# Kernel optimization log

Hardware: AMD Instinct MI355X
Metric: run time of the kernel (lower is better)

Reference implementation:

```python
import jax, jax.numpy as jnp
import numpy as np

B, C, H, W = 4, 1024, 14, 14
L = 80          # num labels / graph nodes
WD = 300        # word embedding dim
INTER = 1024    # semantic intermediary dim
OUT = 2048      # output_dim
TIME_STEP = 3


def setup_inputs() -> dict:
    key = jax.random.key(0)
    ks = jax.random.split(key, 24)
    s = 0.02  # weight scale to keep gates/tanh in sane range
    return {
        "img_feature_map": jax.random.normal(ks[0], (B, C, H, W), jnp.float32),
        "word_embedding": jax.random.normal(ks[1], (L, WD), jnp.float32),
        "adjacency": jax.random.uniform(ks[2], (L, L), jnp.float32) / L,
        "fc1_w": jax.random.normal(ks[3], (INTER, C), jnp.float32) * s,
        "fc2_w": jax.random.normal(ks[4], (INTER, WD), jnp.float32) * s,
        "fc3_w": jax.random.normal(ks[5], (INTER, INTER), jnp.float32) * s,
        "fc3_b": jnp.zeros((INTER,), jnp.float32),
        "fca_w": jax.random.normal(ks[6], (1, INTER), jnp.float32) * s,
        "fca_b": jnp.zeros((1,), jnp.float32),
        "w3": jax.random.normal(ks[7], (C, 2 * C), jnp.float32) * s,
        "b3": jnp.zeros((C,), jnp.float32),
        "u3": jax.random.normal(ks[8], (C, C), jnp.float32) * s,
        "u3b": jnp.zeros((C,), jnp.float32),
        "w4": jax.random.normal(ks[9], (C, 2 * C), jnp.float32) * s,
        "b4": jnp.zeros((C,), jnp.float32),
        "w5": jax.random.normal(ks[10], (C, 2 * C), jnp.float32) * s,
        "b5": jnp.zeros((C,), jnp.float32),
        "u5": jax.random.normal(ks[11], (C, C), jnp.float32) * s,
        "u5b": jnp.zeros((C,), jnp.float32),
        "fco_w": jax.random.normal(ks[12], (OUT, 2 * C), jnp.float32) * s,
        "fco_b": jnp.zeros((OUT,), jnp.float32),
    }


def _semantic(fmap, word_emb, fc1_w, fc2_w, fc3_w, fc3_b, fca_w, fca_b):
    # Faithful to torch: view(-1, C) on a contiguous (B,C,H,W) tensor is a raw
    # row-major reinterpret (NOT a BHWC transpose). jnp.reshape matches.
    b, c, h, w = fmap.shape
    x = fmap.reshape(-1, c)                                   # (B*H*W, C)
    f_wh = x @ fc1_w.T                                        # (N, INTER)
    f_wd = word_emb @ fc2_w.T                                 # (L, INTER)
    lb = jnp.tanh(f_wh[:, None, :] * f_wd[None, :, :])        # (N, L, INTER)
    lb = lb @ fc3_w.T + fc3_b                                 # (N, L, INTER)
    coeff = lb @ fca_w.T + fca_b                              # (N, L, 1)
    coeff = coeff.reshape(b, L, h * w)                        # torch .view semantics
    coeff = jax.nn.softmax(coeff, axis=2)
    coeff = coeff.reshape(b, h, w, L)
    fmap_bhwc = fmap.reshape(b, h, w, c)                      # raw reinterpret, as torch
    return jnp.einsum('bhwl,bhwc->blc', coeff, fmap_bhwc)     # (B, L, C)


def _ggnn(nodes, adj, w3, b3, u3, u3b, w4, b4, w5, b5, u5, u5b):
    for _ in range(TIME_STEP):
        a = jnp.einsum('nm,bmd->bnd', adj, nodes)             # in == out matrix
        av = jnp.concatenate([a, a], axis=-1)                 # (B, L, 2C)
        u3x = nodes @ u3.T + u3b
        z = jax.nn.sigmoid(av @ w3.T + b3 + u3x)
        r = jax.nn.sigmoid(av @ w4.T + b4 + u3x)              # torch bug: reuses fc_eq3_u
        hcand = jnp.tanh(av @ w5.T + b5 + (r * nodes) @ u5.T + u5b)
        nodes = (1.0 - z) * nodes + z * hcand
    return nodes


def reference(img_feature_map, word_embedding, adjacency,
              fc1_w, fc2_w, fc3_w, fc3_b, fca_w, fca_b,
              w3, b3, u3, u3b, w4, b4, w5, b5, u5, u5b,
              fco_w, fco_b):
    g = _semantic(img_feature_map, word_embedding,
                  fc1_w, fc2_w, fc3_w, fc3_b, fca_w, fca_b)   # (B, L, C)
    nodes = _ggnn(g, adjacency, w3, b3, u3, u3b, w4, b4, w5, b5, u5, u5b)
    feat = jnp.concatenate([nodes, g], axis=-1)               # (B, L, 2C)
    out = jnp.tanh(feat @ fco_w.T + fco_b)                    # (B, L, OUT)
    return out
```

## Files before the change

### kernel.cpp

```cpp
#include <hip/hip_runtime.h>
#include <hip/hip_bf16.h>

#define LL 80
#define NPIX 784
#define PBATCH 15680

#define DI __device__ __forceinline__

typedef short s8v __attribute__((ext_vector_type(8)));
typedef short short4v __attribute__((ext_vector_type(4)));
typedef float f32x4 __attribute__((ext_vector_type(4)));

DI float b2f(__hip_bfloat16 x) { return __bfloat162float(x); }
DI float s2f(short h) { return __uint_as_float(((unsigned int)(unsigned short)h) << 16); }

DI short f2b(float x) {
    unsigned int b = __float_as_uint(x);
    b += 0x7fffu + ((b >> 16) & 1u);
    return (short)(b >> 16);
}

template <int F> DI float LD(const void* p, int i) {
    if (F) return ((const float*)p)[i];
    return b2f(((const __hip_bfloat16*)p)[i]);
}

DI float fast_tanh(float x) {
    float e = __expf(2.0f * x);
    return 1.0f - 2.0f / (e + 1.0f);
}
DI float fast_sigmoid(float x) { return 1.0f / (1.0f + __expf(-x)); }

__global__ __launch_bounds__(256) void detect_dtype(const void* probe, int n, int* flag) {
    __shared__ int bad;
    if (threadIdx.x == 0) bad = 0;
    __syncthreads();
    int c = 0;
    for (int i = threadIdx.x; i < n; i += 256) {
        float v = b2f(((const __hip_bfloat16*)probe)[i]);
        if (!(fabsf(v) < 1000.0f)) c++;
    }
    if (c) atomicAdd(&bad, c);
    __syncthreads();
    if (threadIdx.x == 0) *flag = (bad > 8) ? 1 : 0;
}

DI void cvt_part(int f, const void* src, short* __restrict__ dst, int blk, int n) {
    int i0 = (blk * 256 + threadIdx.x) * 4;
    if (i0 >= n) return;
    if (f) {
        float4 v = *(const float4*)((const float*)src + i0);
        short4v o = { f2b(v.x), f2b(v.y), f2b(v.z), f2b(v.w) };
        *(short4v*)(dst + i0) = o;
    } else {
        *(short4v*)(dst + i0) = *(const short4v*)((const short*)src + i0);
    }
}

DI void cvt_pad(int f, const void* src, short* __restrict__ dst, int blk, int n) {
    int i0 = (blk * 256 + threadIdx.x) * 4;
    if (i0 >= n) return;
    int row = i0 / 320;
    int k = i0 - row * 320;
    short4v o = {0, 0, 0, 0};
    if (k < 300) {
        if (f) {
            float4 v = *(const float4*)((const float*)src + row * 300 + k);
            o.x = f2b(v.x); o.y = f2b(v.y); o.z = f2b(v.z); o.w = f2b(v.w);
        } else {
            o = *(const short4v*)((const short*)src + row * 300 + k);
        }
    }
    *(short4v*)(dst + i0) = o;
}

DI void wcat_part(int f, const void* w3, const void* w4, const void* w5, const void* u3,
                  short* __restrict__ wcat, int blk) {
    int i0 = (blk * 256 + threadIdx.x) * 4;
    int nr = i0 >> 10, k = i0 & 1023;
    int j = nr >> 10, r = nr & 1023;
    const void* W = (j == 0) ? w3 : (j == 1) ? w4 : (j == 2) ? w5 : u3;
    float4 v;
    if (j < 3) {
        if (f) {
            float4 x = *(const float4*)((const float*)W + r * 2048 + k);
            float4 y = *(const float4*)((const float*)W + r * 2048 + 1024 + k);
            v.x = x.x + y.x; v.y = x.y + y.y; v.z = x.z + y.z; v.w = x.w + y.w;
        } else {
            const short* Ws = (const short*)W;
            short4v x = *(const short4v*)(Ws + r * 2048 + k);
            short4v y = *(const short4v*)(Ws + r * 2048 + 1024 + k);
            v.x = s2f(x.x) + s2f(y.x); v.y = s2f(x.y) + s2f(y.y);
            v.z = s2f(x.z) + s2f(y.z); v.w = s2f(x.w) + s2f(y.w);
        }
    } else {
        if (f) v = *(const float4*)((const float*)W + r * 1024 + k);
        else {
            short4v x = *(const short4v*)((const short*)W + r * 1024 + k);
            v.x = s2f(x.x); v.y = s2f(x.y); v.z = s2f(x.z); v.w = s2f(x.w);
        }
    }
    short4v o = { f2b(v.x), f2b(v.y), f2b(v.z), f2b(v.w) };
    *(short4v*)(wcat + i0) = o;
}

template <int F>
DI void prep_upart(const void* fc3_w, const void* fca_w,
                   float* __restrict__ u_part, int blk) {
    int kseg = blk >> 4, jseg = blk & 15;
    int k = kseg * 256 + threadIdx.x;
    int j0 = jseg * 64;
    float acc = 0.f;
    for (int j = j0; j < j0 + 64; j++)
        acc += LD<F>(fca_w, j) * LD<F>(fc3_w, j * 1024 + k);
    u_part[jseg * 1024 + k] = acc;
}

template <int F>
DI void prep_c0(const void* fc3_b, const void* fca_w, const void* fca_b,
                float* c0, float* red) {
    float acc = 0.f;
    for (int j = threadIdx.x; j < 1024; j += 256)
        acc += LD<F>(fc3_b, j) * LD<F>(fca_w, j);
    red[threadIdx.x] = acc;
    __syncthreads();
    for (int s = 128; s > 0; s >>= 1) {
        if (threadIdx.x < s) red[threadIdx.x] += red[threadIdx.x + s];
        __syncthreads();
    }
    if (threadIdx.x == 0) {
        float v = red[0] + LD<F>(fca_b, 0);
        c0[0] = v;
        c0[1] = v;
    }
}

__global__ __launch_bounds__(256) void mega_prep(
    const int* flag,
    const void* fmap, const void* fc1_w, const void* u5w,
    const void* w3, const void* w4, const void* w5, const void* u3,
    const void* fc3_w, const void* fc3_b, const void* fca_w, const void* fca_b,
    const void* word, const void* fc2_w,
    short* fmap_b, short* fc1w_b, short* u5w_b, short* wcat_b,
    short* word_b, short* fc2w_b,
    float* u_part, float* c0) {
    __shared__ float red[256];
    int f = *flag;
    int bid = blockIdx.x;
    if      (bid < 784)  cvt_part(f, fmap,  fmap_b, bid,        802816);
    else if (bid < 1808) cvt_part(f, fc1_w, fc1w_b, bid - 784,  1048576);
    else if (bid < 2832) cvt_part(f, u5w,   u5w_b,  bid - 1808, 1048576);
    else if (bid < 6928) wcat_part(f, w3, w4, w5, u3, wcat_b, bid - 2832);
    else if (bid < 6992) {
        if (f) prep_upart<1>(fc3_w, fca_w, u_part, bid - 6928);
        else   prep_upart<0>(fc3_w, fca_w, u_part, bid - 6928);
    } else if (bid == 6992) {
        if (f) prep_c0<1>(fc3_b, fca_w, fca_b, c0, red);
        else   prep_c0<0>(fc3_b, fca_w, fca_b, c0, red);
    }
    else if (bid < 7018) cvt_pad(f, word,  word_b, bid - 6993, 25600);
    else                 cvt_pad(f, fc2_w, fc2w_b, bid - 7018, 327680);
}

__global__ __launch_bounds__(256) void cvt_k(const int* flag, const void* src,
                                             short* __restrict__ dst, int n) {
    cvt_part(*flag, src, dst, blockIdx.x, n);
}

DI void mcore_b(const short* __restrict__ A, int lda,
                const short* __restrict__ B, int ldb,
                float* __restrict__ C, int ldc,
                int M, int kb, int ke, int m0, int n0) {
    __shared__ short As[4][64][8];
    __shared__ short Ws[4][64][8];
    const int tid = threadIdx.x;
    const int wv = tid >> 6, lane = tid & 63;
    const int mA = tid & 63, qA = tid >> 6;
    f32x4 acc[4] = {};

    for (int k0 = kb; k0 < ke; k0 += 32) {
        s8v va = {0,0,0,0,0,0,0,0};
        int gm = m0 + mA;
        if (gm < M) va = *(const s8v*)(A + gm * lda + k0 + 8 * qA);
        *(s8v*)&As[mA >> 4][(mA & 15) | (qA << 4)][0] = va;
        s8v vb = *(const s8v*)(B + (n0 + mA) * ldb + k0 + 8 * qA);
        *(s8v*)&Ws[mA >> 4][(mA & 15) | (qA << 4)][0] = vb;
        __syncthreads();
        s8v af = *(const s8v*)&As[wv][lane][0];
#pragma unroll
        for (int nf = 0; nf < 4; nf++) {
            s8v bf = *(const s8v*)&Ws[nf][lane][0];
            acc[nf] = __builtin_amdgcn_mfma_f32_16x16x32_bf16(af, bf, acc[nf], 0, 0, 0);
        }
        __syncthreads();
    }

    const int q = lane >> 4, cc = lane & 15;
#pragma unroll
    for (int nf = 0; nf < 4; nf++) {
        int n = n0 + 16 * nf + cc;
#pragma unroll
        for (int r = 0; r < 4; r++) {
            int m = m0 + 16 * wv + q * 4 + r;
            if (m < M) C[m * ldc + n] = acc[nf][r];
        }
    }
}

__global__ __launch_bounds__(256) void mfma_sem(
    const short* __restrict__ fmap_b, const short* __restrict__ fc1w_b,
    const short* __restrict__ word_b, const short* __restrict__ fc2w_b,
    const float* __restrict__ u_part, float* __restrict__ u, float* __restrict__ c0,
    float* __restrict__ fhP, float* __restrict__ f_wd) {
    int bid = blockIdx.x;
    if (bid < 416) {
        int z = bid / 208, r = bid % 208;
        int by = r / 16, bx = r % 16;
        mcore_b(fmap_b, 1024, fc1w_b, 1024, fhP + z * 802816, 1024,
                NPIX, z * 512, z * 512 + 512, by * 64, bx * 64);
    } else if (bid < 448) {
        int r = bid - 416;
        int by = r >> 4, bx = r & 15;
        mcore_b(word_b, 320, fc2w_b, 320, f_wd, 1024,
                80, 0, 320, by * 64, bx * 64);
    } else {
        __shared__ float red[256];
        int k = (bid - 448) * 256 + threadIdx.x;
        float a = 0.f;
#pragma unroll
        for (int si = 0; si < 16; si++) a += u_part[si * 1024 + k];
        u[k] = a;
        red[threadIdx.x] = a;
        __syncthreads();
        for (int st = 128; st > 0; st >>= 1) {
            if (threadIdx.x < st) red[threadIdx.x] += red[threadIdx.x + st];
            __syncthreads();
        }
        if (threadIdx.x == 0) atomicAdd(c0 + 1, red[0]);
    }
}

__global__ __launch_bounds__(256) void mfma_gate(
    const short* __restrict__ a_b, const short* __restrict__ nodes_b,
    const short* __restrict__ wcat_b, float* __restrict__ gP) {
    int z = blockIdx.z;
    const short* A = (blockIdx.x >= 48) ? nodes_b : a_b;
    mcore_b(A, 1024, wcat_b, 1024, gP + z * 1310720, 4096,
            320, z * 512, z * 512 + 512, blockIdx.y * 64, blockIdx.x * 64);
}

__global__ __launch_bounds__(256) void mfma_u5(
    const short* __restrict__ rn_b, const short* __restrict__ u5w_b,
    float* __restrict__ u5P) {
    int z = blockIdx.z;
    mcore_b(rn_b, 1024, u5w_b, 1024, u5P + z * 327680, 1024,
            320, z * 256, z * 256 + 256, blockIdx.y * 64, blockIdx.x * 64);
}

__global__ __launch_bounds__(256) void mfma_fin(
    const short* __restrict__ nodes_b, const short* __restrict__ g_b,
    const short* __restrict__ fcow_b, float* __restrict__ finP) {
    int z = blockIdx.z;
    const short* A = z ? (g_b - 1024) : nodes_b;
    mcore_b(A, 1024, fcow_b, 2048, finP + z * 655360, 2048,
            320, z * 1024, z * 1024 + 1024, blockIdx.y * 64, blockIdx.x * 64);
}

__global__ void fin_combine(const int* flag, const float* __restrict__ finP,
                            const void* fco_b, void* out, int n) {
    int i4 = (blockIdx.x * 256 + threadIdx.x) * 4;
    if (i4 >= n) return;
    int c = i4 & 2047;
    float4 p0 = *(const float4*)(finP + i4);
    float4 p1 = *(const float4*)(finP + 655360 + i4);
    int f = *flag;
    float v0 = fast_tanh(p0.x + p1.x + (f ? LD<1>(fco_b, c)   : LD<0>(fco_b, c)));
    float v1 = fast_tanh(p0.y + p1.y + (f ? LD<1>(fco_b, c+1) : LD<0>(fco_b, c+1)));
    float v2 = fast_tanh(p0.z + p1.z + (f ? LD<1>(fco_b, c+2) : LD<0>(fco_b, c+2)));
    float v3 = fast_tanh(p0.w + p1.w + (f ? LD<1>(fco_b, c+3) : LD<0>(fco_b, c+3)));
    if (f) {
        float4 o = {v0, v1, v2, v3};
        *(float4*)((float*)out + i4) = o;
    } else {
        short4v o = { f2b(v0), f2b(v1), f2b(v2), f2b(v3) };
        *(short4v*)((short*)out + i4) = o;
    }
}

__global__ __launch_bounds__(256) void coeff_kernel(
    const float* __restrict__ fhP, const float* __restrict__ f_wd,
    const float* __restrict__ u, const float* __restrict__ c0p,
    float* __restrict__ s) {
    __shared__ float h2s[4][1024];
    __shared__ float us[1024];
    const float K2 = 2.8853900817779268f;
    int t = threadIdx.x;
    int n0 = blockIdx.x * 4;
#pragma unroll
    for (int r = 0; r < 4; r++) {
        int n = n0 + r;
        float4 a0 = *(const float4*)(fhP + n * 1024 + t * 4);
        float4 a1 = *(const float4*)(fhP + 802816 + n * 1024 + t * 4);
        float4 hv = {K2 * (a0.x + a1.x), K2 * (a0.y + a1.y),
                     K2 * (a0.z + a1.z), K2 * (a0.w + a1.w)};
        *(float4*)&h2s[r][t * 4] = hv;
    }
    *(float4*)&us[t * 4] = *(const float4*)(u + t * 4);
    __syncthreads();
    float c0U = c0p[1];
    int wave = t >> 6, lane = t & 63;
    int b = n0 / 196, hw0 = n0 % 196;
    int l0 = blockIdx.y * 20;
    for (int l = l0 + wave; l < l0 + 20; l += 4) {
        const float4* fd4 = (const float4*)(f_wd + l * 1024);
        float p0 = 0.f, p1 = 0.f, p2 = 0.f, p3 = 0.f;
#pragma unroll
        for (int j = 0; j < 4; j++) {
            int idx = lane + j * 64;
            float4 d  = fd4[idx];
            float4 uu = *(const float4*)&us[idx * 4];
            float4 h0 = *(const float4*)&h2s[0][idx * 4];
            float4 h1 = *(const float4*)&h2s[1][idx * 4];
            float4 h2 = *(const float4*)&h2s[2][idx * 4];
            float4 h3 = *(const float4*)&h2s[3][idx * 4];
#define TERM(P, H) \
    P += uu.x * __builtin_amdgcn_rcpf(1.0f + __builtin_amdgcn_exp2f(H.x * d.x)); \
    P += uu.y * __builtin_amdgcn_rcpf(1.0f + __builtin_amdgcn_exp2f(H.y * d.y)); \
    P += uu.z * __builtin_amdgcn_rcpf(1.0f + __builtin_amdgcn_exp2f(H.z * d.z)); \
    P += uu.w * __builtin_amdgcn_rcpf(1.0f + __builtin_amdgcn_exp2f(H.w * d.w));
            TERM(p0, h0) TERM(p1, h1) TERM(p2, h2) TERM(p3, h3)
#undef TERM
        }
        for (int off = 32; off > 0; off >>= 1) {
            p0 += __shfl_down(p0, off);
            p1 += __shfl_down(p1, off);
            p2 += __shfl_down(p2, off);
            p3 += __shfl_down(p3, off);
        }
        if (lane == 0) {
            float* sp = s + b * PBATCH + hw0 * LL + l;
            sp[0]      = c0U - 2.f * p0;
            sp[LL]     = c0U - 2.f * p1;
            sp[2 * LL] = c0U - 2.f * p2;
            sp[3 * LL] = c0U - 2.f * p3;
        }
    }
}

__global__ __launch_bounds__(64) void softmax196(float* __restrict__ s) {
    float* p = s + blockIdx.x * 196;
    int lane = threadIdx.x;
    float v[4];
    float mx = -1e30f;
#pragma unroll
    for (int i = 0; i < 4; i++) {
        int idx = lane + i * 64;
        v[i] = (idx < 196) ? p[idx] : -1e30f;
        mx = fmaxf(mx, v[i]);
    }
    for (int off = 32; off > 0; off >>= 1) mx = fmaxf(mx, __shfl_down(mx, off));
    mx = __shfl(mx, 0);
    float sum = 0.f;
#pragma unroll
    for (int i = 0; i < 4; i++) {
        int idx = lane + i * 64;
        if (idx < 196) { v[i] = __expf(v[i] - mx); sum += v[i]; }
    }
    for (int off = 32; off > 0; off >>= 1) sum += __shfl_down(sum, off);
    sum = __shfl(sum, 0);
    float inv = 1.f / sum;
#pragma unroll
    for (int i = 0; i < 4; i++) {
        int idx = lane + i * 64;
        if (idx < 196) p[idx] = v[i] * inv;
    }
}

__global__ __launch_bounds__(256) void g_kernel(
    const float* __restrict__ s, const short* __restrict__ fmap_b,
    float* __restrict__ nodes, short* __restrict__ nodes_b, short* __restrict__ g_b) {
    int bl = blockIdx.x;
    int b = bl / LL, l = bl % LL;
    __shared__ float co[196];
    for (int i = threadIdx.x; i < 196; i += 256)
        co[i] = s[b * PBATCH + i * LL + l];
    __syncthreads();
    int c4 = threadIdx.x * 4;
    const short* base = fmap_b + b * 196 * 1024 + c4;
    float a0 = 0.f, a1 = 0.f, a2 = 0.f, a3 = 0.f;
    for (int hw = 0; hw < 196; hw++) {
        short4v v = *(const short4v*)(base + hw * 1024);
        float w = co[hw];
        a0 += w * s2f(v.x); a1 += w * s2f(v.y);
        a2 += w * s2f(v.z); a3 += w * s2f(v.w);
    }
    int o = bl * 1024 + c4;
    float4 fa = {a0, a1, a2, a3};
    *(float4*)(nodes + o) = fa;
    short4v bb = { f2b(a0), f2b(a1), f2b(a2), f2b(a3) };
    *(short4v*)(nodes_b + o) = bb;
    *(short4v*)(g_b + o) = bb;
}

template <int F>
DI void adj_core(float* arw, const void* adj, const float* nodes, short* a_b) {
    int bl = blockIdx.x;
    int b = bl / LL, l = bl % LL;
    if (threadIdx.x < LL) arw[threadIdx.x] = LD<F>(adj, l * LL + threadIdx.x);
    __syncthreads();
    int c4 = threadIdx.x * 4;
    const float* nb = nodes + b * LL * 1024 + c4;
    float a0 = 0.f, a1 = 0.f, a2 = 0.f, a3 = 0.f;
    for (int m = 0; m < LL; m++) {
        float am = arw[m];
        float4 nd = *(const float4*)(nb + m * 1024);
        a0 += am * nd.x; a1 += am * nd.y; a2 += am * nd.z; a3 += am * nd.w;
    }
    short4v bb = { f2b(a0), f2b(a1), f2b(a2), f2b(a3) };
    *(short4v*)(a_b + bl * 1024 + c4) = bb;
}

__global__ __launch_bounds__(256) void adj_kernel(
    const int* flag, const void* adj, const float* nodes, short* a_b) {
    __shared__ float arw[LL];
    if (*flag) adj_core<1>(arw, adj, nodes, a_b);
    else       adj_core<0>(arw, adj, nodes, a_b);
}

template <int F>
DI void ew_r_core(const float* gP, const float* nodes,
                  const void* b4, const void* u3b, short* rn_b, int i4) {
    int m = i4 >> 10, c = i4 & 1023;
    int base = m * 4096;
    float4 r0 = *(const float4*)(gP + base + 1024 + c);
    float4 r1 = *(const float4*)(gP + 1310720 + base + 1024 + c);
    float4 x0 = *(const float4*)(gP + base + 3072 + c);
    float4 x1 = *(const float4*)(gP + 1310720 + base + 3072 + c);
    float4 nd = *(const float4*)(nodes + i4);
    short4v o;
    o.x = f2b(fast_sigmoid(r0.x + r1.x + x0.x + x1.x + LD<F>(b4, c)   + LD<F>(u3b, c))   * nd.x);
    o.y = f2b(fast_sigmoid(r0.y + r1.y + x0.y + x1.y + LD<F>(b4, c+1) + LD<F>(u3b, c+1)) * nd.y);
    o.z = f2b(fast_sigmoid(r0.z + r1.z + x0.z + x1.z + LD<F>(b4, c+2) + LD<F>(u3b, c+2)) * nd.z);
    o.w = f2b(fast_sigmoid(r0.w + r1.w + x0.w + x1.w + LD<F>(b4, c+3) + LD<F>(u3b, c+3)) * nd.w);
    *(short4v*)(rn_b + i4) = o;
}

__global__ void ew_r(const int* flag, const float* gP, const float* nodes,
                     const void* b4, const void* u3b, short* rn_b, int n) {
    int i4 = (blockIdx.x * 256 + threadIdx.x) * 4;
    if (i4 >= n) return;
    if (*flag) ew_r_core<1>(gP, nodes, b4, u3b, rn_b, i4);
    else       ew_r_core<0>(gP, nodes, b4, u3b, rn_b, i4);
}

template <int F>
DI void ewu(const float* gP, const float* u5P,
            const void* b3, const void* u3b, const void* b5, const void* u5b,
            float* nodes, short* nodes_b, int i4) {
    int m = i4 >> 10, c = i4 & 1023;
    int base = m * 4096;
    float4 z0 = *(const float4*)(gP + base + c);
    float4 z1 = *(const float4*)(gP + 1310720 + base + c);
    float4 h0 = *(const float4*)(gP + base + 2048 + c);
    float4 h1 = *(const float4*)(gP + 1310720 + base + 2048 + c);
    float4 x0 = *(const float4*)(gP + base + 3072 + c);
    float4 x1 = *(const float4*)(gP + 1310720 + base + 3072 + c);
    float4 u0 = *(const float4*)(u5P + i4);
    float4 u1 = *(const float4*)(u5P + 327680 + i4);
    float4 u2 = *(const float4*)(u5P + 655360 + i4);
    float4 u3v = *(const float4*)(u5P + 983040 + i4);
    float4 nd = *(const float4*)(nodes + i4);
    float4 out;
#define EWU1(CH, CO) { \
    float z = fast_sigmoid(z0.CH + z1.CH + x0.CH + x1.CH + LD<F>(b3, c+CO) + LD<F>(u3b, c+CO)); \
    float h = fast_tanh(h0.CH + h1.CH + u0.CH + u1.CH + u2.CH + u3v.CH + LD<F>(b5, c+CO) + LD<F>(u5b, c+CO)); \
    out.CH = (1.f - z) * nd.CH + z * h; }
    EWU1(x, 0) EWU1(y, 1) EWU1(z, 2) EWU1(w, 3)
#undef EWU1
    *(float4*)(nodes + i4) = out;
    short4v bb = { f2b(out.x), f2b(out.y), f2b(out.z), f2b(out.w) };
    *(short4v*)(nodes_b + i4) = bb;
}

__global__ void ew_upd(const int* flag, const float* gP, const float* u5P,
                       const void* b3, const void* u3b, const void* b5, const void* u5b,
                       float* nodes, short* nodes_b, int n) {
    int i4 = (blockIdx.x * 256 + threadIdx.x) * 4;
    if (i4 >= n) return;
    if (*flag) ewu<1>(gP, u5P, b3, u3b, b5, u5b, nodes, nodes_b, i4);
    else       ewu<0>(gP, u5P, b3, u3b, b5, u5b, nodes, nodes_b, i4);
}

extern "C" void kernel_launch(void* const* d_in, const int* in_sizes, int n_in,
                              void* d_out, int out_size, void* d_ws, size_t ws_size,
                              hipStream_t stream) {
    const void* fmap  = d_in[0];
    const void* word  = d_in[1];
    const void* adjm  = d_in[2];
    const void* fc1_w = d_in[3];
    const void* fc2_w = d_in[4];
    const void* fc3_w = d_in[5];
    const void* fc3_b = d_in[6];
    const void* fca_w = d_in[7];
    const void* fca_b = d_in[8];
    const void* w3    = d_in[9];
    const void* b3    = d_in[10];
    const void* u3    = d_in[11];
    const void* u3b   = d_in[12];
    const void* w4    = d_in[13];
    const void* b4    = d_in[14];
    const void* w5    = d_in[15];
    const void* b5    = d_in[16];
    const void* u5    = d_in[17];
    const void* u5b   = d_in[18];
    const void* fco_w = d_in[19];
    const void* fco_b = d_in[20];

    int*   flag    = (int*)d_ws;
    float* P       = (float*)d_ws + 16;
    float* nodes   = P;                       P += 327680;
    short* nodes_b = (short*)P;               P += 163840;
    short* g_b     = (short*)P;               P += 163840;
    short* a_b     = (short*)P;               P += 163840;
    short* rn_b    = (short*)P;               P += 163840;
    short* u5w_b   = (short*)P;               P += 524288;
    short* wcat_b  = (short*)P;               P += 2097152;
    float* R       = P;
    float* fhP    = R;
    float* f_wd   = R + 1605632;
    float* u_part = f_wd + 81920;
    float* u      = u_part + 16384;
    float* c0     = u + 1024;
    float* s      = c0 + 16;
    short* fmap_b = (short*)(s + 62720);
    short* fc1w_b = fmap_b + 802816;
    short* word_b = fc1w_b + 1048576;
    short* fc2w_b = word_b + 25600;
    float* gP     = R;
    float* u5P    = R + 2621440;
    float* finP   = R;
    short* fcow_b = (short*)(R + 1310720);

    detect_dtype<<<1, 256, 0, stream>>>(fc1_w, 4096, flag);

    mega_prep<<<7338, 256, 0, stream>>>(flag, fmap, fc1_w, u5,
                                        w3, w4, w5, u3,
                                        fc3_w, fc3_b, fca_w, fca_b,
                                        word, fc2_w,
                                        fmap_b, fc1w_b, u5w_b, wcat_b,
                                        word_b, fc2w_b, u_part, c0);

    mfma_sem<<<452, 256, 0, stream>>>(fmap_b, fc1w_b, word_b, fc2w_b,
                                      u_part, u, c0, fhP, f_wd);
    coeff_kernel<<<dim3(196, 4), 256, 0, stream>>>(fhP, f_wd, u, c0, s);
    softmax196<<<320, 64, 0, stream>>>(s);
    g_kernel<<<320, 256, 0, stream>>>(s, fmap_b, nodes, nodes_b, g_b);

    for (int t = 0; t < 3; t++) {
        adj_kernel<<<320, 256, 0, stream>>>(flag, adjm, nodes, a_b);
        mfma_gate<<<dim3(64, 5, 2), 256, 0, stream>>>(a_b, nodes_b, wcat_b, gP);
        ew_r<<<320, 256, 0, stream>>>(flag, gP, nodes, b4, u3b, rn_b, 327680);
        mfma_u5<<<dim3(16, 5, 4), 256, 0, stream>>>(rn_b, u5w_b, u5P);
        ew_upd<<<320, 256, 0, stream>>>(flag, gP, u5P, b3, u3b, b5, u5b,
                                        nodes, nodes_b, 327680);
    }

    cvt_k<<<4096, 256, 0, stream>>>(flag, fco_w, fcow_b, 4194304);
    mfma_fin<<<dim3(32, 5, 2), 256, 0, stream>>>(nodes_b, g_b, fcow_b, finP);
    fin_combine<<<640, 256, 0, stream>>>(flag, finP, fco_b, d_out, 655360);
}
```

Before: 341.2 us.

## Fuse GRU gate GEMM with sigmoid epilogue and concatenate K over adj and nodes

Reorders the combined gate weight so the z and r columns for the same output channels share one tile, and concatenates the adjacency and nodes inputs along K (2048). This lets one GEMM compute full pre-activations and apply sigmoid, biases and r*nodes in its epilogue. It removes the ew_r kernel, the split-K partial buffers and the big gP traffic, and ew_upd gets simpler. It also moves the fco_w bf16 conversion into the prep megakernel when the workspace has room, at the cost of a larger weight buffer and a less parallel gate grid (240 blocks without split-K).

```diff
diff --git a/kernel.cpp b/kernel.cpp
--- a/kernel.cpp
+++ b/kernel.cpp
@@ -24,6 +24,7 @@
     if (F) return ((const float*)p)[i];
     return b2f(((const __hip_bfloat16*)p)[i]);
 }
+DI float LDf(int f, const void* p, int i) { return f ? ((const float*)p)[i] : b2f(((const __hip_bfloat16*)p)[i]); }
 
 DI float fast_tanh(float x) {
     float e = __expf(2.0f * x);
@@ -74,30 +75,49 @@
     *(short4v*)(dst + i0) = o;
 }
 
-DI void wcat_part(int f, const void* w3, const void* w4, const void* w5, const void* u3,
-                  short* __restrict__ wcat, int blk) {
+DI void wcat2_part(int f, const void* w3, const void* w4, const void* w5, const void* u3,
+                   short* __restrict__ wcat, int blk) {
     int i0 = (blk * 256 + threadIdx.x) * 4;
-    int nr = i0 >> 10, k = i0 & 1023;
-    int j = nr >> 10, r = nr & 1023;
-    const void* W = (j == 0) ? w3 : (j == 1) ? w4 : (j == 2) ? w5 : u3;
-    float4 v;
-    if (j < 3) {
-        if (f) {
-            float4 x = *(const float4*)((const float*)W + r * 2048 + k);
-            float4 y = *(const float4*)((const float*)W + r * 2048 + 1024 + k);
-            v.x = x.x + y.x; v.y = x.y + y.y; v.z = x.z + y.z; v.w = x.w + y.w;
+    int j = i0 >> 11, k = i0 & 2047;
+    float4 v = {0.f, 0.f, 0.f, 0.f};
+    if (j < 2048) {
+        int slot = (j >> 4) & 3, cl = j & 15;
+        int c = (j >> 6) * 32 + ((slot >> 1) << 4) + cl;
+        if (k < 1024) {
+            const void* W = (slot & 1) ? w4 : w3;
+            if (f) {
+                float4 x = *(const float4*)((const float*)W + c * 2048 + k);
+                float4 y = *(const float4*)((const float*)W + c * 2048 + 1024 + k);
+                v.x = x.x + y.x; v.y = x.y + y.y; v.z = x.z + y.z; v.w = x.w + y.w;
+            } else {
+                const short* Ws = (const short*)W;
+                short4v x = *(const short4v*)(Ws + c * 2048 + k);
+                short4v y = *(const short4v*)(Ws + c * 2048 + 1024 + k);
+                v.x = s2f(x.x) + s2f(y.x); v.y = s2f(x.y) + s2f(y.y);
+                v.z = s2f(x.z) + s2f(y.z); v.w = s2f(x.w) + s2f(y.w);
+            }
         } else {
-            const short* Ws = (const short*)W;
-            short4v x = *(const short4v*)(Ws + r * 2048 + k);
-            short4v y = *(const short4v*)(Ws + r * 2048 + 1024 + k);
-            v.x = s2f(x.x) + s2f(y.x); v.y = s2f(x.y) + s2f(y.y);
-            v.z = s2f(x.z) + s2f(y.z); v.w = s2f(x.w) + s2f(y.w);
+            int kk = k - 1024;
+            if (f) v = *(const float4*)((const float*)u3 + c * 1024 + kk);
+            else {
+                short4v x = *(const short4v*)((const short*)u3 + c * 1024 + kk);
+                v.x = s2f(x.x); v.y = s2f(x.y); v.z = s2f(x.z); v.w = s2f(x.w);
+            }
         }
     } else {
-        if (f) v = *(const float4*)((const float*)W + r * 1024 + k);
-        else {
-            short4v x = *(const short4v*)((const short*)W + r * 1024 + k);
-            v.x = s2f(x.x); v.y = s2f(x.y); v.z = s2f(x.z); v.w = s2f(x.w);
+        int c = j - 2048;
+        if (k < 1024) {
+            if (f) {
+                float4 x = *(const float4*)((const float*)w5 + c * 2048 + k);
+                float4 y = *(const float4*)((const float*)w5 + c * 2048 + 1024 + k);
+                v.x = x.x + y.x; v.y = x.y + y.y; v.z = x.z + y.z; v.w = x.w + y.w;
+            } else {
+                const short* Ws = (const short*)w5;
+                short4v x = *(const short4v*)(Ws + c * 2048 + k);
+                short4v y = *(const short4v*)(Ws + c * 2048 + 1024 + k);
+                v.x = s2f(x.x) + s2f(y.x); v.y = s2f(x.y) + s2f(y.y);
+                v.z = s2f(x.z) + s2f(y.z); v.w = s2f(x.w) + s2f(y.w);
+            }
         }
     }
     short4v o = { f2b(v.x), f2b(v.y), f2b(v.z), f2b(v.w) };
@@ -140,9 +160,9 @@
     const void* fmap, const void* fc1_w, const void* u5w,
     const void* w3, const void* w4, const void* w5, const void* u3,
     const void* fc3_w, const void* fc3_b, const void* fca_w, const void* fca_b,
-    const void* word, const void* fc2_w,
+    const void* word, const void* fc2_w, const void* fco_w,
     short* fmap_b, short* fc1w_b, short* u5w_b, short* wcat_b,
-    short* word_b, short* fc2w_b,
+    short* word_b, short* fc2w_b, short* fcow_b,
     float* u_part, float* c0) {
     __shared__ float red[256];
     int f = *flag;
@@ -150,16 +170,17 @@
     if      (bid < 784)  cvt_part(f, fmap,  fmap_b, bid,        802816);
     else if (bid < 1808) cvt_part(f, fc1_w, fc1w_b, bid - 784,  1048576);
     else if (bid < 2832) cvt_part(f, u5w,   u5w_b,  bid - 1808, 1048576);
-    else if (bid < 6928) wcat_part(f, w3, w4, w5, u3, wcat_b, bid - 2832);
-    else if (bid < 6992) {
-        if (f) prep_upart<1>(fc3_w, fca_w, u_part, bid - 6928);
-        else   prep_upart<0>(fc3_w, fca_w, u_part, bid - 6928);
-    } else if (bid == 6992) {
+    else if (bid < 8976) wcat2_part(f, w3, w4, w5, u3, wcat_b, bid - 2832);
+    else if (bid < 9040) {
+        if (f) prep_upart<1>(fc3_w, fca_w, u_part, bid - 8976);
+        else   prep_upart<0>(fc3_w, fca_w, u_part, bid - 8976);
+    } else if (bid == 9040) {
         if (f) prep_c0<1>(fc3_b, fca_w, fca_b, c0, red);
         else   prep_c0<0>(fc3_b, fca_w, fca_b, c0, red);
     }
-    else if (bid < 7018) cvt_pad(f, word,  word_b, bid - 6993, 25600);
-    else                 cvt_pad(f, fc2_w, fc2w_b, bid - 7018, 327680);
+    else if (bid < 9066) cvt_pad(f, word,  word_b, bid - 9041, 25600);
+    else if (bid < 9386) cvt_pad(f, fc2_w, fc2w_b, bid - 9066, 327680);
+    else                 cvt_part(f, fco_w, fcow_b, bid - 9386, 4194304);
 }
 
 __global__ __launch_bounds__(256) void cvt_k(const int* flag, const void* src,
@@ -240,13 +261,75 @@
     }
 }
 
-__global__ __launch_bounds__(256) void mfma_gate(
+__global__ __launch_bounds__(256) void mfma_gateF(
+    const int* flag,
     const short* __restrict__ a_b, const short* __restrict__ nodes_b,
-    const short* __restrict__ wcat_b, float* __restrict__ gP) {
-    int z = blockIdx.z;
-    const short* A = (blockIdx.x >= 48) ? nodes_b : a_b;
-    mcore_b(A, 1024, wcat_b, 1024, gP + z * 1310720, 4096,
-            320, z * 512, z * 512 + 512, blockIdx.y * 64, blockIdx.x * 64);
+    const short* __restrict__ wcat_b, const float* __restrict__ nodes,
+    const void* b3, const void* b4, const void* u3b,
+    const void* b5, const void* u5b,
+    float* __restrict__ zs, float* __restrict__ hp, short* __restrict__ rn_b) {
+    __shared__ short As[4][64][8];
+    __shared__ short Ws[4][64][8];
+    const int tid = threadIdx.x;
+    const int wv = tid >> 6, lane = tid & 63;
+    const int mA = tid & 63, qA = tid >> 6;
+    const int bn = blockIdx.x;
+    const int m0 = blockIdx.y * 64;
+    const int n0 = bn * 64;
+    const int ke = (bn < 32) ? 2048 : 1024;
+    f32x4 acc[4] = {};
+
+    for (int k0 = 0; k0 < ke; k0 += 32) {
+        const short* Arow = (k0 < 1024)
+            ? (a_b + (m0 + mA) * 1024 + k0)
+            : (nodes_b + (m0 + mA) * 1024 + (k0 - 1024));
+        s8v va = *(const s8v*)(Arow + 8 * qA);
+        *(s8v*)&As[mA >> 4][(mA & 15) | (qA << 4)][0] = va;
+        s8v vb = *(const s8v*)(wcat_b + (n0 + mA) * 2048 + k0 + 8 * qA);
+        *(s8v*)&Ws[mA >> 4][(mA & 15) | (qA << 4)][0] = vb;
+        __syncthreads();
+        s8v af = *(const s8v*)&As[wv][lane][0];
+#pragma unroll
+        for (int nf = 0; nf < 4; nf++) {
+            s8v bf = *(const s8v*)&Ws[nf][lane][0];
+            acc[nf] = __builtin_amdgcn_mfma_f32_16x16x32_bf16(af, bf, acc[nf], 0, 0, 0);
+        }
+        __syncthreads();
+    }
+
+    const int q = lane >> 4, cc = lane & 15;
+    const int f = *flag;
+    if (bn < 32) {
+        int c0c = bn * 32 + cc;
+        int c1c = c0c + 16;
+        float bz0 = LDf(f, b3, c0c) + LDf(f, u3b, c0c);
+        float br0 = LDf(f, b4, c0c) + LDf(f, u3b, c0c);
+        float bz1 = LDf(f, b3, c1c) + LDf(f, u3b, c1c);
+        float br1 = LDf(f, b4, c1c) + LDf(f, u3b, c1c);
+#pragma unroll
+        for (int r = 0; r < 4; r++) {
+            int m = m0 + 16 * wv + q * 4 + r;
+            float z0v = fast_sigmoid(acc[0][r] + bz0);
+            float r0v = fast_sigmoid(acc[1][r] + br0);
+            float z1v = fast_sigmoid(acc[2][r] + bz1);
+            float r1v = fast_sigmoid(acc[3][r] + br1);
+            zs[m * 1024 + c0c] = z0v;
+            zs[m * 1024 + c1c] = z1v;
+            rn_b[m * 1024 + c0c] = f2b(r0v * nodes[m * 1024 + c0c]);
+            rn_b[m * 1024 + c1c] = f2b(r1v * nodes[m * 1024 + c1c]);
+        }
+    } else {
+#pragma unroll
+        for (int nf = 0; nf < 4; nf++) {
+            int c = (bn - 32) * 64 + 16 * nf + cc;
+            float bb = LDf(f, b5, c) + LDf(f, u5b, c);
+#pragma unroll
+            for (int r = 0; r < 4; r++) {
+                int m = m0 + 16 * wv + q * 4 + r;
+                hp[m * 1024 + c] = acc[nf][r] + bb;
+            }
+        }
+    }
 }
 
 __global__ __launch_bounds__(256) void mfma_u5(
@@ -427,68 +510,26 @@
     else       adj_core<0>(arw, adj, nodes, a_b);
 }
 
-template <int F>
-DI void ew_r_core(const float* gP, const float* nodes,
-                  const void* b4, const void* u3b, short* rn_b, int i4) {
-    int m = i4 >> 10, c = i4 & 1023;
-    int base = m * 4096;
-    float4 r0 = *(const float4*)(gP + base + 1024 + c);
-    float4 r1 = *(const float4*)(gP + 1310720 + base + 1024 + c);
-    float4 x0 = *(const float4*)(gP + base + 3072 + c);
-    float4 x1 = *(const float4*)(gP + 1310720 + base + 3072 + c);
-    float4 nd = *(const float4*)(nodes + i4);
-    short4v o;
-    o.x = f2b(fast_sigmoid(r0.x + r1.x + x0.x + x1.x + LD<F>(b4, c)   + LD<F>(u3b, c))   * nd.x);
-    o.y = f2b(fast_sigmoid(r0.y + r1.y + x0.y + x1.y + LD<F>(b4, c+1) + LD<F>(u3b, c+1)) * nd.y);
-    o.z = f2b(fast_sigmoid(r0.z + r1.z + x0.z + x1.z + LD<F>(b4, c+2) + LD<F>(u3b, c+2)) * nd.z);
-    o.w = f2b(fast_sigmoid(r0.w + r1.w + x0.w + x1.w + LD<F>(b4, c+3) + LD<F>(u3b, c+3)) * nd.w);
-    *(short4v*)(rn_b + i4) = o;
-}
-
-__global__ void ew_r(const int* flag, const float* gP, const float* nodes,
-                     const void* b4, const void* u3b, short* rn_b, int n) {
+__global__ void ew_upd(const float* __restrict__ zs, const float* __restrict__ hp,
+                       const float* __restrict__ u5P,
+                       float* __restrict__ nodes, short* __restrict__ nodes_b, int n) {
     int i4 = (blockIdx.x * 256 + threadIdx.x) * 4;
     if (i4 >= n) return;
-    if (*flag) ew_r_core<1>(gP, nodes, b4, u3b, rn_b, i4);
-    else       ew_r_core<0>(gP, nodes, b4, u3b, rn_b, i4);
-}
-
-template <int F>
-DI void ewu(const float* gP, const float* u5P,
-            const void* b3, const void* u3b, const void* b5, const void* u5b,
-            float* nodes, short* nodes_b, int i4) {
-    int m = i4 >> 10, c = i4 & 1023;
-    int base = m * 4096;
-    float4 z0 = *(const float4*)(gP + base + c);
-    float4 z1 = *(const float4*)(gP + 1310720 + base + c);
-    float4 h0 = *(const float4*)(gP + base + 2048 + c);
-    float4 h1 = *(const float4*)(gP + 1310720 + base + 2048 + c);
-    float4 x0 = *(const float4*)(gP + base + 3072 + c);
-    float4 x1 = *(const float4*)(gP + 1310720 + base + 3072 + c);
+    float4 zv = *(const float4*)(zs + i4);
+    float4 hv = *(const float4*)(hp + i4);
     float4 u0 = *(const float4*)(u5P + i4);
     float4 u1 = *(const float4*)(u5P + 327680 + i4);
     float4 u2 = *(const float4*)(u5P + 655360 + i4);
     float4 u3v = *(const float4*)(u5P + 983040 + i4);
     float4 nd = *(const float4*)(nodes + i4);
     float4 out;
-#define EWU1(CH, CO) { \
-    float z = fast_sigmoid(z0.CH + z1.CH + x0.CH + x1.CH + LD<F>(b3, c+CO) + LD<F>(u3b, c+CO)); \
-    float h = fast_tanh(h0.CH + h1.CH + u0.CH + u1.CH + u2.CH + u3v.CH + LD<F>(b5, c+CO) + LD<F>(u5b, c+CO)); \
-    out.CH = (1.f - z) * nd.CH + z * h; }
-    EWU1(x, 0) EWU1(y, 1) EWU1(z, 2) EWU1(w, 3)
-#undef EWU1
+    out.x = (1.f - zv.x) * nd.x + zv.x * fast_tanh(hv.x + u0.x + u1.x + u2.x + u3v.x);
+    out.y = (1.f - zv.y) * nd.y + zv.y * fast_tanh(hv.y + u0.y + u1.y + u2.y + u3v.y);
+    out.z = (1.f - zv.z) * nd.z + zv.z * fast_tanh(hv.z + u0.z + u1.z + u2.z + u3v.z);
+    out.w = (1.f - zv.w) * nd.w + zv.w * fast_tanh(hv.w + u0.w + u1.w + u2.w + u3v.w);
     *(float4*)(nodes + i4) = out;
     short4v bb = { f2b(out.x), f2b(out.y), f2b(out.z), f2b(out.w) };
     *(short4v*)(nodes_b + i4) = bb;
-}
-
-__global__ void ew_upd(const int* flag, const float* gP, const float* u5P,
-                       const void* b3, const void* u3b, const void* b5, const void* u5b,
-                       float* nodes, short* nodes_b, int n) {
-    int i4 = (blockIdx.x * 256 + threadIdx.x) * 4;
-    if (i4 >= n) return;
-    if (*flag) ewu<1>(gP, u5P, b3, u3b, b5, u5b, nodes, nodes_b, i4);
-    else       ewu<0>(gP, u5P, b3, u3b, b5, u5b, nodes, nodes_b, i4);
 }
 
 extern "C" void kernel_launch(void* const* d_in, const int* in_sizes, int n_in,
@@ -524,7 +565,12 @@
     short* a_b     = (short*)P;               P += 163840;
     short* rn_b    = (short*)P;               P += 163840;
     short* u5w_b   = (short*)P;               P += 524288;
-    short* wcat_b  = (short*)P;               P += 2097152;
+    short* wcat_b  = (short*)P;               P += 3145728;
+    size_t base_f = 16 + 327680 + 163840*4 + 524288 + 3145728;
+    size_t need_ded = (base_f + 2097152 + 2870032) * 4;
+    bool fco_ded = ws_size >= need_ded;
+    short* fcow_ded = (short*)P;
+    if (fco_ded) P += 2097152;
     float* R       = P;
     float* fhP    = R;
     float* f_wd   = R + 1605632;
@@ -536,19 +582,19 @@
     short* fc1w_b = fmap_b + 802816;
     short* word_b = fc1w_b + 1048576;
     short* fc2w_b = word_b + 25600;
-    float* gP     = R;
-    float* u5P    = R + 2621440;
+    float* zs     = R;
+    float* hp     = R + 327680;
+    float* u5P    = R + 655360;
     float* finP   = R;
-    short* fcow_b = (short*)(R + 1310720);
+    short* fcow_b = fco_ded ? fcow_ded : wcat_b;
 
     detect_dtype<<<1, 256, 0, stream>>>(fc1_w, 4096, flag);
 
-    mega_prep<<<7338, 256, 0, stream>>>(flag, fmap, fc1_w, u5,
-                                        w3, w4, w5, u3,
-                                        fc3_w, fc3_b, fca_w, fca_b,
-                                        word, fc2_w,
-                                        fmap_b, fc1w_b, u5w_b, wcat_b,
-                                        word_b, fc2w_b, u_part, c0);
+    mega_prep<<<fco_ded ? 13482 : 9386, 256, 0, stream>>>(
+        flag, fmap, fc1_w, u5, w3, w4, w5, u3,
+        fc3_w, fc3_b, fca_w, fca_b, word, fc2_w, fco_w,
+        fmap_b, fc1w_b, u5w_b, wcat_b, word_b, fc2w_b, fcow_ded,
+        u_part, c0);
 
     mfma_sem<<<452, 256, 0, stream>>>(fmap_b, fc1w_b, word_b, fc2w_b,
                                       u_part, u, c0, fhP, f_wd);
@@ -558,14 +604,15 @@
 
     for (int t = 0; t < 3; t++) {
         adj_kernel<<<320, 256, 0, stream>>>(flag, adjm, nodes, a_b);
-        mfma_gate<<<dim3(64, 5, 2), 256, 0, stream>>>(a_b, nodes_b, wcat_b, gP);
-        ew_r<<<320, 256, 0, stream>>>(flag, gP, nodes, b4, u3b, rn_b, 327680);
+        mfma_gateF<<<dim3(48, 5), 256, 0, stream>>>(flag, a_b, nodes_b, wcat_b,
+                                                    nodes, b3, b4, u3b, b5, u5b,
+                                                    zs, hp, rn_b);
         mfma_u5<<<dim3(16, 5, 4), 256, 0, stream>>>(rn_b, u5w_b, u5P);
-        ew_upd<<<320, 256, 0, stream>>>(flag, gP, u5P, b3, u3b, b5, u5b,
-                                        nodes, nodes_b, 327680);
-    }
-
-    cvt_k<<<4096, 256, 0, stream>>>(flag, fco_w, fcow_b, 4194304);
+        ew_upd<<<320, 256, 0, stream>>>(zs, hp, u5P, nodes, nodes_b, 327680);
+    }
+
+    if (!fco_ded)
+        cvt_k<<<4096, 256, 0, stream>>>(flag, fco_w, fcow_b, 4194304);
     mfma_fin<<<dim3(32, 5, 2), 256, 0, stream>>>(nodes_b, g_b, fcow_b, finP);
     fin_combine<<<640, 256, 0, stream>>>(flag, finP, fco_b, d_out, 655360);
 }
```

After: 390.7 us. 14.5% more time.

## Fuse final GEMM split-K with bias-tanh epilogue and fold fco_w conversion into prep

Applied to the files above, without the earlier changes.

The fco_w bf16 conversion moves into the mega_prep launch with a dedicated workspace buffer, which removes one kernel launch. The final projection becomes a single kernel that runs the whole K=2048 reduction, switching its A source from nodes to g at the midpoint, and applies bias and tanh in the epilogue. This drops the split-K partial buffer and the separate combine kernel. In exchange the final GEMM has only 160 blocks, each with a K loop twice as long, so it exposes less parallelism.

```diff
diff --git a/kernel.cpp b/kernel.cpp
--- a/kernel.cpp
+++ b/kernel.cpp
@@ -24,6 +24,7 @@
     if (F) return ((const float*)p)[i];
     return b2f(((const __hip_bfloat16*)p)[i]);
 }
+DI float LDf(int f, const void* p, int i) { return f ? ((const float*)p)[i] : b2f(((const __hip_bfloat16*)p)[i]); }
 
 DI float fast_tanh(float x) {
     float e = __expf(2.0f * x);
@@ -140,9 +141,9 @@
     const void* fmap, const void* fc1_w, const void* u5w,
     const void* w3, const void* w4, const void* w5, const void* u3,
     const void* fc3_w, const void* fc3_b, const void* fca_w, const void* fca_b,
-    const void* word, const void* fc2_w,
+    const void* word, const void* fc2_w, const void* fco_w,
     short* fmap_b, short* fc1w_b, short* u5w_b, short* wcat_b,
-    short* word_b, short* fc2w_b,
+    short* word_b, short* fc2w_b, short* fcow_b,
     float* u_part, float* c0) {
     __shared__ float red[256];
     int f = *flag;
@@ -159,12 +160,8 @@
         else   prep_c0<0>(fc3_b, fca_w, fca_b, c0, red);
     }
     else if (bid < 7018) cvt_pad(f, word,  word_b, bid - 6993, 25600);
-    else                 cvt_pad(f, fc2_w, fc2w_b, bid - 7018, 327680);
-}
-
-__global__ __launch_bounds__(256) void cvt_k(const int* flag, const void* src,
-                                             short* __restrict__ dst, int n) {
-    cvt_part(*flag, src, dst, blockIdx.x, n);
+    else if (bid < 7338) cvt_pad(f, fc2_w, fc2w_b, bid - 7018, 327680);
+    else                 cvt_part(f, fco_w, fcow_b, bid - 7338, 4194304);
 }
 
 DI void mcore_b(const short* __restrict__ A, int lda,
@@ -204,6 +201,33 @@
             int m = m0 + 16 * wv + q * 4 + r;
             if (m < M) C[m * ldc + n] = acc[nf][r];
         }
+    }
+}
+
+DI void mcore_acc(const short* __restrict__ Aa, const short* __restrict__ Ab, int ksw,
+                  int lda, const short* __restrict__ B, int ldb,
+                  int kb, int ke, int m0, int n0, f32x4* acc) {
+    __shared__ short As[4][64][8];
+    __shared__ short Ws[4][64][8];
+    const int tid = threadIdx.x;
+    const int wv = tid >> 6, lane = tid & 63;
+    const int mA = tid & 63, qA = tid >> 6;
+
+    for (int k0 = kb; k0 < ke; k0 += 32) {
+        const short* Ar = (k0 < ksw) ? (Aa + (m0 + mA) * lda + k0)
+                                     : (Ab + (m0 + mA) * lda + (k0 - ksw));
+        s8v va = *(const s8v*)(Ar + 8 * qA);
+        *(s8v*)&As[mA >> 4][(mA & 15) | (qA << 4)][0] = va;
+        s8v vb = *(const s8v*)(B + (n0 + mA) * ldb + k0 + 8 * qA);
+        *(s8v*)&Ws[mA >> 4][(mA & 15) | (qA << 4)][0] = vb;
+        __syncthreads();
+        s8v af = *(const s8v*)&As[wv][lane][0];
+#pragma unroll
+        for (int nf = 0; nf < 4; nf++) {
+            s8v bf = *(const s8v*)&Ws[nf][lane][0];
+            acc[nf] = __builtin_amdgcn_mfma_f32_16x16x32_bf16(af, bf, acc[nf], 0, 0, 0);
+        }
+        __syncthreads();
     }
 }
 
@@ -257,33 +281,28 @@
             320, z * 256, z * 256 + 256, blockIdx.y * 64, blockIdx.x * 64);
 }
 
-__global__ __launch_bounds__(256) void mfma_fin(
+__global__ __launch_bounds__(256) void mfma_finC(
+    const int* flag,
     const short* __restrict__ nodes_b, const short* __restrict__ g_b,
-    const short* __restrict__ fcow_b, float* __restrict__ finP) {
-    int z = blockIdx.z;
-    const short* A = z ? (g_b - 1024) : nodes_b;
-    mcore_b(A, 1024, fcow_b, 2048, finP + z * 655360, 2048,
-            320, z * 1024, z * 1024 + 1024, blockIdx.y * 64, blockIdx.x * 64);
-}
-
-__global__ void fin_combine(const int* flag, const float* __restrict__ finP,
-                            const void* fco_b, void* out, int n) {
-    int i4 = (blockIdx.x * 256 + threadIdx.x) * 4;
-    if (i4 >= n) return;
-    int c = i4 & 2047;
-    float4 p0 = *(const float4*)(finP + i4);
-    float4 p1 = *(const float4*)(finP + 655360 + i4);
-    int f = *flag;
-    float v0 = fast_tanh(p0.x + p1.x + (f ? LD<1>(fco_b, c)   : LD<0>(fco_b, c)));
-    float v1 = fast_tanh(p0.y + p1.y + (f ? LD<1>(fco_b, c+1) : LD<0>(fco_b, c+1)));
-    float v2 = fast_tanh(p0.z + p1.z + (f ? LD<1>(fco_b, c+2) : LD<0>(fco_b, c+2)));
-    float v3 = fast_tanh(p0.w + p1.w + (f ? LD<1>(fco_b, c+3) : LD<0>(fco_b, c+3)));
-    if (f) {
-        float4 o = {v0, v1, v2, v3};
-        *(float4*)((float*)out + i4) = o;
-    } else {
-        short4v o = { f2b(v0), f2b(v1), f2b(v2), f2b(v3) };
-        *(short4v*)((short*)out + i4) = o;
+    const short* __restrict__ fcow_b, const void* fco_b, void* out) {
+    f32x4 acc[4] = {};
+    int m0 = blockIdx.y * 64, n0 = blockIdx.x * 64;
+    mcore_acc(nodes_b, g_b, 1024, 1024, fcow_b, 2048, 0, 2048, m0, n0, acc);
+    const int tid = threadIdx.x;
+    const int wv = tid >> 6, lane = tid & 63;
+    const int q = lane >> 4, cc = lane & 15;
+    const int f = *flag;
+#pragma unroll
+    for (int nf = 0; nf < 4; nf++) {
+        int n = n0 + 16 * nf + cc;
+        float bb = LDf(f, fco_b, n);
+#pragma unroll
+        for (int r = 0; r < 4; r++) {
+            int m = m0 + 16 * wv + q * 4 + r;
+            float v = fast_tanh(acc[nf][r] + bb);
+            if (f) ((float*)out)[m * 2048 + n] = v;
+            else   ((short*)out)[m * 2048 + n] = f2b(v);
+        }
     }
 }
 
@@ -525,6 +544,7 @@
     short* rn_b    = (short*)P;               P += 163840;
     short* u5w_b   = (short*)P;               P += 524288;
     short* wcat_b  = (short*)P;               P += 2097152;
+    short* fcow_b  = (short*)P;               P += 2097152;
     float* R       = P;
     float* fhP    = R;
     float* f_wd   = R + 1605632;
@@ -538,17 +558,14 @@
     short* fc2w_b = word_b + 25600;
     float* gP     = R;
     float* u5P    = R + 2621440;
-    float* finP   = R;
-    short* fcow_b = (short*)(R + 1310720);
 
     detect_dtype<<<1, 256, 0, stream>>>(fc1_w, 4096, flag);
 
-    mega_prep<<<7338, 256, 0, stream>>>(flag, fmap, fc1_w, u5,
-                                        w3, w4, w5, u3,
-                                        fc3_w, fc3_b, fca_w, fca_b,
-                                        word, fc2_w,
-                                        fmap_b, fc1w_b, u5w_b, wcat_b,
-                                        word_b, fc2w_b, u_part, c0);
+    mega_prep<<<11434, 256, 0, stream>>>(
+        flag, fmap, fc1_w, u5, w3, w4, w5, u3,
+        fc3_w, fc3_b, fca_w, fca_b, word, fc2_w, fco_w,
+        fmap_b, fc1w_b, u5w_b, wcat_b, word_b, fc2w_b, fcow_b,
+        u_part, c0);
 
     mfma_sem<<<452, 256, 0, stream>>>(fmap_b, fc1w_b, word_b, fc2w_b,
                                       u_part, u, c0, fhP, f_wd);
@@ -565,7 +582,6 @@
                                         nodes, nodes_b, 327680);
     }
 
-    cvt_k<<<4096, 256, 0, stream>>>(flag, fco_w, fcow_b, 4194304);
-    mfma_fin<<<dim3(32, 5, 2), 256, 0, stream>>>(nodes_b, g_b, fcow_b, finP);
-    fin_combine<<<640, 256, 0, stream>>>(flag, finP, fco_b, d_out, 655360);
-}
+    mfma_finC<<<dim3(32, 5), 256, 0, stream>>>(flag, nodes_b, g_b, fcow_b,
+                                               fco_b, d_out);
+}
```

New measurement: 353.9 us. 1.04x slower.

## Prefetch next K-slice in GEMM core, fold fco_w conversion into prep, split final GEMM

Applied to the files above, without the earlier changes.

The shared MFMA GEMM core now loads the next 32-wide K slice of A and B into registers before the barrier, overlapping global loads with the MFMA work on the current slice. The fco_w bf16 conversion moves out of its own launch into the mega_prep kernel, with its own workspace buffer so it no longer aliases the scratch region. The final GEMM is split four ways along K instead of two, which doubles the block count, and fin_combine now sums four partials. This trades more partial-sum traffic and a larger prep launch for fewer launches and better latency hiding.

```diff
diff --git a/kernel.cpp b/kernel.cpp
--- a/kernel.cpp
+++ b/kernel.cpp
@@ -24,6 +24,7 @@
     if (F) return ((const float*)p)[i];
     return b2f(((const __hip_bfloat16*)p)[i]);
 }
+DI float LDf(int f, const void* p, int i) { return f ? ((const float*)p)[i] : b2f(((const __hip_bfloat16*)p)[i]); }
 
 DI float fast_tanh(float x) {
     float e = __expf(2.0f * x);
@@ -140,9 +141,9 @@
     const void* fmap, const void* fc1_w, const void* u5w,
     const void* w3, const void* w4, const void* w5, const void* u3,
     const void* fc3_w, const void* fc3_b, const void* fca_w, const void* fca_b,
-    const void* word, const void* fc2_w,
+    const void* word, const void* fc2_w, const void* fco_w,
     short* fmap_b, short* fc1w_b, short* u5w_b, short* wcat_b,
-    short* word_b, short* fc2w_b,
+    short* word_b, short* fc2w_b, short* fcow_b,
     float* u_part, float* c0) {
     __shared__ float red[256];
     int f = *flag;
@@ -159,12 +160,8 @@
         else   prep_c0<0>(fc3_b, fca_w, fca_b, c0, red);
     }
     else if (bid < 7018) cvt_pad(f, word,  word_b, bid - 6993, 25600);
-    else                 cvt_pad(f, fc2_w, fc2w_b, bid - 7018, 327680);
-}
-
-__global__ __launch_bounds__(256) void cvt_k(const int* flag, const void* src,
-                                             short* __restrict__ dst, int n) {
-    cvt_part(*flag, src, dst, blockIdx.x, n);
+    else if (bid < 7338) cvt_pad(f, fc2_w, fc2w_b, bid - 7018, 327680);
+    else                 cvt_part(f, fco_w, fcow_b, bid - 7338, 4194304);
 }
 
 DI void mcore_b(const short* __restrict__ A, int lda,
@@ -176,15 +173,23 @@
     const int tid = threadIdx.x;
     const int wv = tid >> 6, lane = tid & 63;
     const int mA = tid & 63, qA = tid >> 6;
+    const int gm = m0 + mA;
+    const short* Arow = A + gm * lda + 8 * qA;
+    const short* Brow = B + (n0 + mA) * ldb + 8 * qA;
     f32x4 acc[4] = {};
 
+    s8v va = {0,0,0,0,0,0,0,0};
+    if (gm < M) va = *(const s8v*)(Arow + kb);
+    s8v vb = *(const s8v*)(Brow + kb);
+
     for (int k0 = kb; k0 < ke; k0 += 32) {
-        s8v va = {0,0,0,0,0,0,0,0};
-        int gm = m0 + mA;
-        if (gm < M) va = *(const s8v*)(A + gm * lda + k0 + 8 * qA);
         *(s8v*)&As[mA >> 4][(mA & 15) | (qA << 4)][0] = va;
-        s8v vb = *(const s8v*)(B + (n0 + mA) * ldb + k0 + 8 * qA);
         *(s8v*)&Ws[mA >> 4][(mA & 15) | (qA << 4)][0] = vb;
+        int k1 = k0 + 32;
+        if (k1 < ke) {
+            if (gm < M) va = *(const s8v*)(Arow + k1);
+            vb = *(const s8v*)(Brow + k1);
+        }
         __syncthreads();
         s8v af = *(const s8v*)&As[wv][lane][0];
 #pragma unroll
@@ -261,9 +266,9 @@
     const short* __restrict__ nodes_b, const short* __restrict__ g_b,
     const short* __restrict__ fcow_b, float* __restrict__ finP) {
     int z = blockIdx.z;
-    const short* A = z ? (g_b - 1024) : nodes_b;
+    const short* A = (z < 2) ? nodes_b : (g_b - 1024);
     mcore_b(A, 1024, fcow_b, 2048, finP + z * 655360, 2048,
-            320, z * 1024, z * 1024 + 1024, blockIdx.y * 64, blockIdx.x * 64);
+            320, z * 512, z * 512 + 512, blockIdx.y * 64, blockIdx.x * 64);
 }
 
 __global__ void fin_combine(const int* flag, const float* __restrict__ finP,
@@ -273,11 +278,13 @@
     int c = i4 & 2047;
     float4 p0 = *(const float4*)(finP + i4);
     float4 p1 = *(const float4*)(finP + 655360 + i4);
+    float4 p2 = *(const float4*)(finP + 1310720 + i4);
+    float4 p3 = *(const float4*)(finP + 1966080 + i4);
     int f = *flag;
-    float v0 = fast_tanh(p0.x + p1.x + (f ? LD<1>(fco_b, c)   : LD<0>(fco_b, c)));
-    float v1 = fast_tanh(p0.y + p1.y + (f ? LD<1>(fco_b, c+1) : LD<0>(fco_b, c+1)));
-    float v2 = fast_tanh(p0.z + p1.z + (f ? LD<1>(fco_b, c+2) : LD<0>(fco_b, c+2)));
-    float v3 = fast_tanh(p0.w + p1.w + (f ? LD<1>(fco_b, c+3) : LD<0>(fco_b, c+3)));
+    float v0 = fast_tanh(p0.x + p1.x + p2.x + p3.x + LDf(f, fco_b, c));
+    float v1 = fast_tanh(p0.y + p1.y + p2.y + p3.y + LDf(f, fco_b, c + 1));
+    float v2 = fast_tanh(p0.z + p1.z + p2.z + p3.z + LDf(f, fco_b, c + 2));
+    float v3 = fast_tanh(p0.w + p1.w + p2.w + p3.w + LDf(f, fco_b, c + 3));
     if (f) {
         float4 o = {v0, v1, v2, v3};
         *(float4*)((float*)out + i4) = o;
@@ -525,6 +532,7 @@
     short* rn_b    = (short*)P;               P += 163840;
     short* u5w_b   = (short*)P;               P += 524288;
     short* wcat_b  = (short*)P;               P += 2097152;
+    short* fcow_b  = (short*)P;               P += 2097152;
     float* R       = P;
     float* fhP    = R;
     float* f_wd   = R + 1605632;
@@ -539,16 +547,14 @@
     float* gP     = R;
     float* u5P    = R + 2621440;
     float* finP   = R;
-    short* fcow_b = (short*)(R + 1310720);
 
     detect_dtype<<<1, 256, 0, stream>>>(fc1_w, 4096, flag);
 
-    mega_prep<<<7338, 256, 0, stream>>>(flag, fmap, fc1_w, u5,
-                                        w3, w4, w5, u3,
-                                        fc3_w, fc3_b, fca_w, fca_b,
-                                        word, fc2_w,
-                                        fmap_b, fc1w_b, u5w_b, wcat_b,
-                                        word_b, fc2w_b, u_part, c0);
+    mega_prep<<<11434, 256, 0, stream>>>(
+        flag, fmap, fc1_w, u5, w3, w4, w5, u3,
+        fc3_w, fc3_b, fca_w, fca_b, word, fc2_w, fco_w,
+        fmap_b, fc1w_b, u5w_b, wcat_b, word_b, fc2w_b, fcow_b,
+        u_part, c0);
 
     mfma_sem<<<452, 256, 0, stream>>>(fmap_b, fc1w_b, word_b, fc2w_b,
                                       u_part, u, c0, fhP, f_wd);
@@ -565,7 +571,6 @@
                                         nodes, nodes_b, 327680);
     }
 
-    cvt_k<<<4096, 256, 0, stream>>>(flag, fco_w, fcow_b, 4194304);
-    mfma_fin<<<dim3(32, 5, 2), 256, 0, stream>>>(nodes_b, g_b, fcow_b, finP);
+    mfma_fin<<<dim3(32, 5, 4), 256, 0, stream>>>(nodes_b, g_b, fcow_b, finP);
     fin_combine<<<640, 256, 0, stream>>>(flag, finP, fco_b, d_out, 655360);
 }
```

Result: faster. 325.4 us (-4.6%).
